# Optimization experiments

Measured on AMD Instinct MI355X. Metric: run time of the kernel, lower is better.

Reference implementation:

```python
import jax, jax.numpy as jnp
import numpy as np

N_DF = 96      # number of deep-filtered frequency bins
BASE = 0       # base_bin
N_ORDER = 5    # FIR taps along time


def setup_inputs() -> dict:
    key = jax.random.key(0)
    k1, k2 = jax.random.split(key)
    B, T, F = 8, 3000, 481
    # complex spectrogram stored as [..., 2] = (real, imag)
    spec = jax.random.normal(k1, (B, T, F, 2), dtype=jnp.float32)
    # per-frame complex FIR coefficients: [..., :N_ORDER]=real, [..., N_ORDER:]=imag
    coef = jax.random.normal(k2, (B, T, N_DF, 2 * N_ORDER), dtype=jnp.float32)
    return {"spec": spec, "coef": coef}


def _df_forward(spec, coef):
    T = spec.shape[1]
    # narrow to the deep-filter band
    xr = spec[:, :, BASE:BASE + N_DF, 0]  # [B,T,N_DF]
    xi = spec[:, :, BASE:BASE + N_DF, 1]
    # causal pad along time (ConstantPad2d((0,0,n_order-1,0)))
    pad = ((0, 0), (N_ORDER - 1, 0), (0, 0))
    pr = jnp.pad(xr, pad)
    pi = jnp.pad(xi, pad)
    # unfold(time, n_order, 1) -> [B,T,N_DF,N_ORDER]; loop is over fixed tap count
    ur = jnp.stack([pr[:, k:k + T] for k in range(N_ORDER)], axis=-1)
    ui = jnp.stack([pi[:, k:k + T] for k in range(N_ORDER)], axis=-1)
    cr = coef[..., :N_ORDER]
    ci = coef[..., N_ORDER:]
    # complex sliding dot product: sum_k u[k] * c[k]
    fr = jnp.sum(ur * cr - ui * ci, axis=-1)  # [B,T,N_DF]
    fi = jnp.sum(ur * ci + ui * cr, axis=-1)
    out = spec.at[:, :, BASE:BASE + N_DF, 0].set(fr)
    out = out.at[:, :, BASE:BASE + N_DF, 1].set(fi)
    return out


def reference(spec, coef):
    return _df_forward(spec, coef)
```

## Files before the change

### kernel.cpp

```cpp
#include <hip/hip_runtime.h>


#define BN    8
#define TN    3000
#define FN    481
#define NDF   96
#define NORD  5
#define ROWF  (FN * 2)
#define THALF (TN / 2)
#define NPASS (FN - NDF)

typedef float f2 __attribute__((ext_vector_type(2)));

__global__ __launch_bounds__(256) void df_kernel(const float* __restrict__ spec,
                                                 const float* __restrict__ coef,
                                                 float* __restrict__ out) {
    const int i = blockIdx.x * blockDim.x + threadIdx.x;
    const int nFiltP = BN * THALF * NDF;
    const int nPassP = BN * THALF * NPASS;
    if (i >= nFiltP + nPassP) return;

    if (i < nFiltP) {
        const int f   = i % NDF;
        const int bth = i / NDF;
        const int th  = bth % THALF;
        const int b   = bth / THALF;
        const int t0  = th * 2;
        const long bt0   = (long)b * TN + t0;
        const long base0 = bt0 * ROWF + f * 2;

        const f2* cp = (const f2*)(coef + (bt0 * NDF + f) * (2 * NORD));
        const f2* cq = cp + NDF * NORD;
        const f2 c0a = cp[0], c0b = cp[1], c0c = cp[2], c0d = cp[3], c0e = cp[4];
        const f2 c1a = cq[0], c1b = cq[1], c1c = cq[2], c1d = cq[3], c1e = cq[4];

        const float* sp = spec + base0;
        f2 x0, x1, x2, x3, x4, x5;
        if (t0 >= NORD - 1) {
            x0 = *(const f2*)(sp - 4 * ROWF);
            x1 = *(const f2*)(sp - 3 * ROWF);
            x2 = *(const f2*)(sp - 2 * ROWF);
            x3 = *(const f2*)(sp - 1 * ROWF);
            x4 = *(const f2*)(sp);
            x5 = *(const f2*)(sp + 1 * ROWF);
        } else {
            const f2 z = {0.f, 0.f};
            x0 = (t0 >= 4) ? *(const f2*)(sp - 4 * ROWF) : z;
            x1 = (t0 >= 3) ? *(const f2*)(sp - 3 * ROWF) : z;
            x2 = (t0 >= 2) ? *(const f2*)(sp - 2 * ROWF) : z;
            x3 = (t0 >= 1) ? *(const f2*)(sp - 1 * ROWF) : z;
            x4 = *(const f2*)(sp);
            x5 = *(const f2*)(sp + 1 * ROWF);
        }

        float fr0, fi0, fr1, fi1;
        {
            const float cr0 = c0a.x, cr1 = c0a.y, cr2 = c0b.x, cr3 = c0b.y, cr4 = c0c.x;
            const float ci0 = c0c.y, ci1 = c0d.x, ci2 = c0d.y, ci3 = c0e.x, ci4 = c0e.y;
            fr0 = x0.x*cr0 - x0.y*ci0; fi0 = x0.x*ci0 + x0.y*cr0;
            fr0 += x1.x*cr1 - x1.y*ci1; fi0 += x1.x*ci1 + x1.y*cr1;
            fr0 += x2.x*cr2 - x2.y*ci2; fi0 += x2.x*ci2 + x2.y*cr2;
            fr0 += x3.x*cr3 - x3.y*ci3; fi0 += x3.x*ci3 + x3.y*cr3;
            fr0 += x4.x*cr4 - x4.y*ci4; fi0 += x4.x*ci4 + x4.y*cr4;
        }
        {
            const float cr0 = c1a.x, cr1 = c1a.y, cr2 = c1b.x, cr3 = c1b.y, cr4 = c1c.x;
            const float ci0 = c1c.y, ci1 = c1d.x, ci2 = c1d.y, ci3 = c1e.x, ci4 = c1e.y;
            fr1 = x1.x*cr0 - x1.y*ci0; fi1 = x1.x*ci0 + x1.y*cr0;
            fr1 += x2.x*cr1 - x2.y*ci1; fi1 += x2.x*ci1 + x2.y*cr1;
            fr1 += x3.x*cr2 - x3.y*ci2; fi1 += x3.x*ci2 + x3.y*cr2;
            fr1 += x4.x*cr3 - x4.y*ci3; fi1 += x4.x*ci3 + x4.y*cr3;
            fr1 += x5.x*cr4 - x5.y*ci4; fi1 += x5.x*ci4 + x5.y*cr4;
        }

        const f2 o0 = {fr0, fi0};
        const f2 o1 = {fr1, fi1};
        __builtin_nontemporal_store(o0, (f2*)(out + base0));
        __builtin_nontemporal_store(o1, (f2*)(out + base0 + ROWF));
    } else {
        const int j   = i - nFiltP;
        const int fp  = NDF + j % NPASS;
        const int bth = j / NPASS;
        const int th  = bth % THALF;
        const int b   = bth / THALF;
        const long bt0  = (long)b * TN + th * 2;
        const long idx0 = bt0 * ROWF + fp * 2;

        const f2 a = *(const f2*)(spec + idx0);
        const f2 c = *(const f2*)(spec + idx0 + ROWF);
        __builtin_nontemporal_store(a, (f2*)(out + idx0));
        __builtin_nontemporal_store(c, (f2*)(out + idx0 + ROWF));
    }
}

extern "C" void kernel_launch(void* const* d_in, const int* in_sizes, int n_in,
                              void* d_out, int out_size, void* d_ws, size_t ws_size,
                              hipStream_t stream) {
    const float* spec = (const float*)d_in[0];
    const float* coef = (const float*)d_in[1];
    float* out = (float*)d_out;

    const int nTot = BN * THALF * NDF + BN * THALF * NPASS;
    const int block = 256;
    const int grid = (nTot + block - 1) / block;
    df_kernel<<<grid, block, 0, stream>>>(spec, coef, out);
}
```

Before: 232.7 us.

## Split passthrough into vectorized full copy kernel plus band-only filter kernel

```diff
diff --git a/kernel.cpp b/kernel.cpp
--- a/kernel.cpp
+++ b/kernel.cpp
@@ -8,89 +8,81 @@
 #define NORD  5
 #define ROWF  (FN * 2)
 #define THALF (TN / 2)
-#define NPASS (FN - NDF)
 
 typedef float f2 __attribute__((ext_vector_type(2)));
 
-__global__ __launch_bounds__(256) void df_kernel(const float* __restrict__ spec,
-                                                 const float* __restrict__ coef,
-                                                 float* __restrict__ out) {
+__global__ __launch_bounds__(256) void copy_kernel(const float4* __restrict__ in,
+                                                   float4* __restrict__ out,
+                                                   int n4) {
+    const int base = blockIdx.x * (256 * 4) + threadIdx.x;
+    #pragma unroll
+    for (int k = 0; k < 4; ++k) {
+        const int idx = base + k * 256;
+        if (idx < n4) out[idx] = in[idx];
+    }
+}
+
+__global__ __launch_bounds__(256) void df_filt_kernel(const float* __restrict__ spec,
+                                                      const float* __restrict__ coef,
+                                                      float* __restrict__ out) {
     const int i = blockIdx.x * blockDim.x + threadIdx.x;
     const int nFiltP = BN * THALF * NDF;
-    const int nPassP = BN * THALF * NPASS;
-    if (i >= nFiltP + nPassP) return;
+    if (i >= nFiltP) return;
 
-    if (i < nFiltP) {
-        const int f   = i % NDF;
-        const int bth = i / NDF;
-        const int th  = bth % THALF;
-        const int b   = bth / THALF;
-        const int t0  = th * 2;
-        const long bt0   = (long)b * TN + t0;
-        const long base0 = bt0 * ROWF + f * 2;
+    const int f   = i % NDF;
+    const int bth = i / NDF;
+    const int th  = bth % THALF;
+    const int b   = bth / THALF;
+    const int t0  = th * 2;
+    const int bt0   = b * TN + t0;
+    const int base0 = bt0 * ROWF + f * 2;
 
-        const f2* cp = (const f2*)(coef + (bt0 * NDF + f) * (2 * NORD));
-        const f2* cq = cp + NDF * NORD;
-        const f2 c0a = cp[0], c0b = cp[1], c0c = cp[2], c0d = cp[3], c0e = cp[4];
-        const f2 c1a = cq[0], c1b = cq[1], c1c = cq[2], c1d = cq[3], c1e = cq[4];
+    const f2* cp = (const f2*)(coef + (bt0 * NDF + f) * (2 * NORD));
+    const f2* cq = cp + NDF * NORD;
+    const f2 c0a = cp[0], c0b = cp[1], c0c = cp[2], c0d = cp[3], c0e = cp[4];
+    const f2 c1a = cq[0], c1b = cq[1], c1c = cq[2], c1d = cq[3], c1e = cq[4];
 
-        const float* sp = spec + base0;
-        f2 x0, x1, x2, x3, x4, x5;
-        if (t0 >= NORD - 1) {
-            x0 = *(const f2*)(sp - 4 * ROWF);
-            x1 = *(const f2*)(sp - 3 * ROWF);
-            x2 = *(const f2*)(sp - 2 * ROWF);
-            x3 = *(const f2*)(sp - 1 * ROWF);
-            x4 = *(const f2*)(sp);
-            x5 = *(const f2*)(sp + 1 * ROWF);
-        } else {
-            const f2 z = {0.f, 0.f};
-            x0 = (t0 >= 4) ? *(const f2*)(sp - 4 * ROWF) : z;
-            x1 = (t0 >= 3) ? *(const f2*)(sp - 3 * ROWF) : z;
-            x2 = (t0 >= 2) ? *(const f2*)(sp - 2 * ROWF) : z;
-            x3 = (t0 >= 1) ? *(const f2*)(sp - 1 * ROWF) : z;
-            x4 = *(const f2*)(sp);
-            x5 = *(const f2*)(sp + 1 * ROWF);
-        }
+    const float* sp = spec + base0;
+    f2 x0, x1, x2, x3, x4, x5;
+    if (t0 >= NORD - 1) {
+        x0 = *(const f2*)(sp - 4 * ROWF);
+        x1 = *(const f2*)(sp - 3 * ROWF);
+        x2 = *(const f2*)(sp - 2 * ROWF);
+        x3 = *(const f2*)(sp - 1 * ROWF);
+        x4 = *(const f2*)(sp);
+        x5 = *(const f2*)(sp + 1 * ROWF);
+    } else {
+        const f2 z = {0.f, 0.f};
+        x0 = (t0 >= 4) ? *(const f2*)(sp - 4 * ROWF) : z;
+        x1 = (t0 >= 3) ? *(const f2*)(sp - 3 * ROWF) : z;
+        x2 = (t0 >= 2) ? *(const f2*)(sp - 2 * ROWF) : z;
+        x3 = (t0 >= 1) ? *(const f2*)(sp - 1 * ROWF) : z;
+        x4 = *(const f2*)(sp);
+        x5 = *(const f2*)(sp + 1 * ROWF);
+    }
 
-        float fr0, fi0, fr1, fi1;
-        {
-            const float cr0 = c0a.x, cr1 = c0a.y, cr2 = c0b.x, cr3 = c0b.y, cr4 = c0c.x;
-            const float ci0 = c0c.y, ci1 = c0d.x, ci2 = c0d.y, ci3 = c0e.x, ci4 = c0e.y;
-            fr0 = x0.x*cr0 - x0.y*ci0; fi0 = x0.x*ci0 + x0.y*cr0;
-            fr0 += x1.x*cr1 - x1.y*ci1; fi0 += x1.x*ci1 + x1.y*cr1;
-            fr0 += x2.x*cr2 - x2.y*ci2; fi0 += x2.x*ci2 + x2.y*cr2;
-            fr0 += x3.x*cr3 - x3.y*ci3; fi0 += x3.x*ci3 + x3.y*cr3;
-            fr0 += x4.x*cr4 - x4.y*ci4; fi0 += x4.x*ci4 + x4.y*cr4;
-        }
-        {
-            const float cr0 = c1a.x, cr1 = c1a.y, cr2 = c1b.x, cr3 = c1b.y, cr4 = c1c.x;
-            const float ci0 = c1c.y, ci1 = c1d.x, ci2 = c1d.y, ci3 = c1e.x, ci4 = c1e.y;
-            fr1 = x1.x*cr0 - x1.y*ci0; fi1 = x1.x*ci0 + x1.y*cr0;
-            fr1 += x2.x*cr1 - x2.y*ci1; fi1 += x2.x*ci1 + x2.y*cr1;
-            fr1 += x3.x*cr2 - x3.y*ci2; fi1 += x3.x*ci2 + x3.y*cr2;
-            fr1 += x4.x*cr3 - x4.y*ci3; fi1 += x4.x*ci3 + x4.y*cr3;
-            fr1 += x5.x*cr4 - x5.y*ci4; fi1 += x5.x*ci4 + x5.y*cr4;
-        }
+    float fr0, fi0, fr1, fi1;
+    {
+        const float cr0 = c0a.x, cr1 = c0a.y, cr2 = c0b.x, cr3 = c0b.y, cr4 = c0c.x;
+        const float ci0 = c0c.y, ci1 = c0d.x, ci2 = c0d.y, ci3 = c0e.x, ci4 = c0e.y;
+        fr0 = x0.x*cr0 - x0.y*ci0; fi0 = x0.x*ci0 + x0.y*cr0;
+        fr0 += x1.x*cr1 - x1.y*ci1; fi0 += x1.x*ci1 + x1.y*cr1;
+        fr0 += x2.x*cr2 - x2.y*ci2; fi0 += x2.x*ci2 + x2.y*cr2;
+        fr0 += x3.x*cr3 - x3.y*ci3; fi0 += x3.x*ci3 + x3.y*cr3;
+        fr0 += x4.x*cr4 - x4.y*ci4; fi0 += x4.x*ci4 + x4.y*cr4;
+    }
+    {
+        const float cr0 = c1a.x, cr1 = c1a.y, cr2 = c1b.x, cr3 = c1b.y, cr4 = c1c.x;
+        const float ci0 = c1c.y, ci1 = c1d.x, ci2 = c1d.y, ci3 = c1e.x, ci4 = c1e.y;
+        fr1 = x1.x*cr0 - x1.y*ci0; fi1 = x1.x*ci0 + x1.y*cr0;
+        fr1 += x2.x*cr1 - x2.y*ci1; fi1 += x2.x*ci1 + x2.y*cr1;
+        fr1 += x3.x*cr2 - x3.y*ci2; fi1 += x3.x*ci2 + x3.y*cr2;
+        fr1 += x4.x*cr3 - x4.y*ci3; fi1 += x4.x*ci3 + x4.y*cr3;
+        fr1 += x5.x*cr4 - x5.y*ci4; fi1 += x5.x*ci4 + x5.y*cr4;
+    }
 
-        const f2 o0 = {fr0, fi0};
-        const f2 o1 = {fr1, fi1};
-        __builtin_nontemporal_store(o0, (f2*)(out + base0));
-        __builtin_nontemporal_store(o1, (f2*)(out + base0 + ROWF));
-    } else {
-        const int j   = i - nFiltP;
-        const int fp  = NDF + j % NPASS;
-        const int bth = j / NPASS;
-        const int th  = bth % THALF;
-        const int b   = bth / THALF;
-        const long bt0  = (long)b * TN + th * 2;
-        const long idx0 = bt0 * ROWF + fp * 2;
-
-        const f2 a = *(const f2*)(spec + idx0);
-        const f2 c = *(const f2*)(spec + idx0 + ROWF);
-        __builtin_nontemporal_store(a, (f2*)(out + idx0));
-        __builtin_nontemporal_store(c, (f2*)(out + idx0 + ROWF));
-    }
+    *(f2*)(out + base0)        = (f2){fr0, fi0};
+    *(f2*)(out + base0 + ROWF) = (f2){fr1, fi1};
 }
 
 extern "C" void kernel_launch(void* const* d_in, const int* in_sizes, int n_in,
@@ -100,8 +92,11 @@
     const float* coef = (const float*)d_in[1];
     float* out = (float*)d_out;
 
-    const int nTot = BN * THALF * NDF + BN * THALF * NPASS;
-    const int block = 256;
-    const int grid = (nTot + block - 1) / block;
-    df_kernel<<<grid, block, 0, stream>>>(spec, coef, out);
+    const int n4 = BN * TN * FN * 2 / 4;
+    const int gridA = (n4 + 1024 - 1) / 1024;
+    copy_kernel<<<gridA, 256, 0, stream>>>((const float4*)spec, (float4*)out, n4);
+
+    const int nFiltP = BN * THALF * NDF;
+    const int gridB = (nFiltP + 255) / 256;
+    df_filt_kernel<<<gridB, 256, 0, stream>>>(spec, coef, out);
 }
```

Result: faster. 227.1 us (-2.4%).
